# Optimization experiments

Hardware: AMD Instinct MI355X
Metric: run time of the kernel (lower is better)

The kernel has to match this reference:

```python
import jax, jax.numpy as jnp
import numpy as np

# --- module hyperparameters (init_kwargs) ---
IN_CH = 512
OUT_CH = 512
NUM_HEADS = 8
MODES = 64
LQ = 4096
LKV = 4096
E = IN_CH // NUM_HEADS      # per-head input dim = 64
EO = OUT_CH // NUM_HEADS    # per-head output dim = 64
B = 16

# mode_select_method='lowest' -> lowest-frequency modes, sorted (deterministic)
INDEX_Q = np.arange(min(MODES, LQ // 2))    # [Mq]
INDEX_KV = np.arange(min(MODES, LKV // 2))  # [Mkv]
SCALE = 1.0 / (IN_CH * OUT_CH)


def setup_inputs() -> dict:
    key = jax.random.key(0)
    kq, kk, kv, kw1, kw2 = jax.random.split(key, 5)
    return {
        "q": jax.random.normal(kq, (B, LQ, NUM_HEADS, E), jnp.float32),
        "k": jax.random.normal(kk, (B, LKV, NUM_HEADS, E), jnp.float32),
        "v": jax.random.normal(kv, (B, LKV, NUM_HEADS, E), jnp.float32),
        "weights1": SCALE * jax.random.normal(kw1, (NUM_HEADS, E, EO, len(INDEX_Q)), jnp.float32),
        "weights2": SCALE * jax.random.normal(kw2, (NUM_HEADS, E, EO, len(INDEX_Q)), jnp.float32),
    }


def reference(q, k, v, weights1, weights2):
    # q: [B, Lq, H, E]; k, v: [B, Lkv, H, E] (v is computed-but-unused in the
    # original forward; kept for signature fidelity).
    Bq, Lq, H, _ = q.shape
    xq = jnp.transpose(q, (0, 2, 3, 1))  # [B, H, E, Lq]
    xk = jnp.transpose(k, (0, 2, 3, 1))  # [B, H, E, Lkv]

    # rFFT along time, then gather the selected frequency modes
    xq_ft = jnp.fft.rfft(xq, axis=-1)[..., INDEX_Q]    # [B, H, E, Mq] complex
    xk_ft = jnp.fft.rfft(xk, axis=-1)[..., INDEX_KV]   # [B, H, E, Mkv] complex

    # complex cross-attention over modes (contract head-dim E)
    xqk = jnp.einsum('bhex,bhey->bhxy', xq_ft, xk_ft)  # [B, H, Mq, Mkv]
    # tanh applied independently to real/imag parts (as in compl activation)
    xqk = jax.lax.complex(jnp.tanh(xqk.real), jnp.tanh(xqk.imag))

    xqkv = jnp.einsum('bhxy,bhey->bhex', xqk, xk_ft)   # [B, H, E, Mq]

    w = jax.lax.complex(weights1, weights2)            # [H, E, EO, Mq]
    xqkvw = jnp.einsum('bhex,heox->bhox', xqkv, w)     # [B, H, EO, Mq]

    # scatter selected modes back into full half-spectrum, inverse FFT
    out_ft = jnp.zeros((Bq, H, EO, Lq // 2 + 1), jnp.complex64)
    out_ft = out_ft.at[..., INDEX_Q].set(xqkvw)
    out = jnp.fft.irfft(out_ft, n=Lq, axis=-1)         # [B, H, EO, Lq]

    out = jnp.transpose(out, (0, 3, 1, 2)) / (IN_CH * OUT_CH)  # [B, Lq, H, EO]
    return out
```

## Files before the change

kernel.cpp:

```cpp
#include <hip/hip_runtime.h>
#include <math.h>


constexpr float TWOPI_L = 1.5339807878856412e-3f;

typedef __attribute__((ext_vector_type(8))) short short8;
typedef __attribute__((ext_vector_type(4))) float f32x4;

__device__ __forceinline__ unsigned short f2bf(float f) {
    unsigned int u = __builtin_bit_cast(unsigned int, f);
    unsigned int r = (u + 0x7fffu + ((u >> 16) & 1u)) >> 16;
    return (unsigned short)r;
}
__device__ __forceinline__ float bf2f(unsigned short h) {
    unsigned int u = ((unsigned int)h) << 16;
    return __builtin_bit_cast(float, u);
}
__device__ __forceinline__ unsigned int cvtpk(float a, float b) {
    unsigned int r;
    asm("v_cvt_pk_bf16_f32 %0, %1, %2" : "=v"(r) : "v"(a), "v"(b));
    return r;
}
__device__ __forceinline__ void gld16(const float* g, void* l) {
    __builtin_amdgcn_global_load_lds(
        (const __attribute__((address_space(1))) void*)(g),
        (__attribute__((address_space(3))) void*)(l),
        16, 0, 0);
}
#define MSKR(r) (((((r) & 7)) << 1) | ((((r) >> 3)) & 1))

__global__ __launch_bounds__(256) void k0_twiddle(unsigned short* __restrict__ Whi,
                                                  unsigned short* __restrict__ Wlo) {
    const int idx = blockIdx.x * 256 + threadIdx.x;
    const int kt = idx >> 9;
    const int rb = (idx >> 6) & 7;
    const int l15 = (idx >> 2) & 15;
    const int lg = idx & 3;
    const int r_tab = rb * 16 + l15;
    int m, c;
    if (r_tab < 64) { m = (r_tab >> 1) * 2;              c = r_tab & 1; }
    else            { m = (((r_tab - 64) >> 1) * 2) + 1; c = r_tab & 1; }
    const int addr = (kt * 8 + rb) * 512 + l15 * 32 + lg * 8;
    unsigned short hbuf[8], lbuf[8];
#pragma unroll
    for (int j = 0; j < 8; ++j) {
        const int t = kt * 32 + lg * 8 + j;
        float sv, cv;
        sincosf((float)((m * t) & 4095) * TWOPI_L, &sv, &cv);
        const float v = c ? -sv : cv;
        const unsigned short hi = f2bf(v);
        hbuf[j] = hi;
        lbuf[j] = f2bf(v - bf2f(hi));
    }
    *(uint4*)(Whi + addr) = *(uint4*)hbuf;
    *(uint4*)(Wlo + addr) = *(uint4*)lbuf;
}

__global__ __launch_bounds__(256) void k0_basis(unsigned short* __restrict__ basis) {
    const int idx = blockIdx.x * 256 + threadIdx.x;
    const int p0 = idx << 2;
    const int t = p0 >> 6;
    unsigned int pk[4];
#pragma unroll
    for (int j = 0; j < 4; ++j) {
        const int m = (p0 & 63) + j;
        float sv, cv;
        sincosf((float)((m * t) & 4095) * TWOPI_L, &sv, &cv);
        const float c = (m == 0) ? 1.0f : 2.0f * cv;
        const float s = (m == 0) ? 0.0f : -2.0f * sv;
        pk[j] = (unsigned int)f2bf(c) | ((unsigned int)f2bf(s) << 16);
    }
    *(uint4*)(basis + (size_t)t * 128u + ((p0 & 63) << 1)) =
        make_uint4(pk[0], pk[1], pk[2], pk[3]);
}

__global__ __launch_bounds__(256, 2) void k1_mfma(const float* __restrict__ q,
                                                  const float* __restrict__ kin,
                                                  const unsigned short* __restrict__ Whi,
                                                  const unsigned short* __restrict__ Wlo,
                                                  float* __restrict__ Xq, float* __restrict__ Xk,
                                                  float* __restrict__ Pq, float* __restrict__ Pk)
{
    __shared__ float raw[3][64][64];
    __shared__ unsigned short xT[4][64][40];

    const int tid = threadIdx.x;
    const int bid = blockIdx.x;
    const int bh = bid >> 3, src = (bid >> 2) & 1, seg = bid & 3;
    const int b = bh >> 3, h = bh & 7;
    const float* __restrict__ x = src ? kin : q;
    const float* xb = x + (size_t)b * 2097152u + (size_t)h * 64u;

    const int wid = tid >> 6, lane = tid & 63;
    const int l15 = lane & 15, lg = lane >> 4;
    const int fp = (tid & 15) * 2;
    const int eqs = tid >> 4;
    const int sel = (wid >> 1) * 2;

    f32x4 acc[2][4];
#pragma unroll
    for (int mt = 0; mt < 2; ++mt)
#pragma unroll
        for (int nt = 0; nt < 4; ++nt)
            acc[mt][nt] = (f32x4){0.f, 0.f, 0.f, 0.f};

#define K1_STAGE(IT, BUF) do {                                                  \
    const int t0_ = (seg * 16 + ((IT) & 15)) * 32;                              \
    float* rbase_ = &raw[BUF][0][0];                                            \
    _Pragma("unroll")                                                           \
    for (int j = 0; j < 4; ++j) {                                               \
        const int c_ = wid * 4 + j;                                             \
        const int rl_ = 4 * c_ + (lane >> 4);                                   \
        const int t_ = t0_ + (rl_ & 31) + ((rl_ >> 5) << 11);                   \
        const int sq_ = (lane & 15) ^ MSKR(rl_);                                \
        gld16(xb + (size_t)t_ * 512u + (size_t)(sq_ * 4), rbase_ + c_ * 256);   \
    }                                                                           \
} while (0)

#define K1_ALOAD(IT, AH, AL) do {                                               \
    const int ksg_ = seg * 16 + ((IT) & 15);                                    \
    _Pragma("unroll")                                                           \
    for (int mt = 0; mt < 2; ++mt) {                                            \
        const size_t o_ = (size_t)((ksg_ * 8 + (wid * 2 + mt)) * 512 + l15 * 32 + lg * 8); \
        AH[mt] = *(const short8*)(Whi + o_);                                    \
        AL[mt] = *(const short8*)(Wlo + o_);                                    \
    }                                                                           \
} while (0)

#define K1_CONVERT(BUF) do {                                                    \
    const float* rb_ = &raw[BUF][0][0];                                         \
    float rs[16];                                                               \
    *(f32x4*)&rs[0]  = *(const f32x4*)(rb_ + (fp     ) * 64 + ((eqs ^ MSKR(fp))      * 4)); \
    *(f32x4*)&rs[4]  = *(const f32x4*)(rb_ + (fp + 1 ) * 64 + ((eqs ^ MSKR(fp + 1))  * 4)); \
    *(f32x4*)&rs[8]  = *(const f32x4*)(rb_ + (fp + 32) * 64 + ((eqs ^ MSKR(fp + 32)) * 4)); \
    *(f32x4*)&rs[12] = *(const f32x4*)(rb_ + (fp + 33) * 64 + ((eqs ^ MSKR(fp + 33)) * 4)); \
    _Pragma("unroll")                                                           \
    for (int ee = 0; ee < 4; ++ee) {                                            \
        const float a0 = rs[ee], a1 = rs[4 + ee];                               \
        const float c0 = rs[8 + ee], c1 = rs[12 + ee];                          \
        const float xp0 = a0 + c0, xp1 = a1 + c1;                               \
        const float xm0 = a0 - c0, xm1 = a1 - c1;                               \
        const int e_ = eqs * 4 + ee;                                            \
        const unsigned int php = cvtpk(xp0, xp1);                               \
        const float ph0 = __builtin_bit_cast(float, php << 16);                 \
        const float ph1 = __builtin_bit_cast(float, php & 0xffff0000u);         \
        const unsigned int plp = cvtpk(xp0 - ph0, xp1 - ph1);                   \
        const unsigned int mhp = cvtpk(xm0, xm1);                               \
        const float mh0 = __builtin_bit_cast(float, mhp << 16);                 \
        const float mh1 = __builtin_bit_cast(float, mhp & 0xffff0000u);         \
        const unsigned int mlp = cvtpk(xm0 - mh0, xm1 - mh1);                   \
        *(unsigned int*)&xT[0][e_][fp] = php;                                   \
        *(unsigned int*)&xT[1][e_][fp] = plp;                                   \
        *(unsigned int*)&xT[2][e_][fp] = mhp;                                   \
        *(unsigned int*)&xT[3][e_][fp] = mlp;                                   \
    }                                                                           \
} while (0)

#define K1_MFMA(AH, AL) do {                                                    \
    const unsigned short* sh = &xT[sel][0][0];                                  \
    const unsigned short* sl = &xT[sel + 1][0][0];                              \
    _Pragma("unroll")                                                           \
    for (int nt = 0; nt < 4; ++nt) {                                            \
        const int ri = (nt * 16 + l15) * 40 + 8 * lg;                           \
        const short8 Bh = *(const short8*)(sh + ri);                            \
        const short8 Bl = *(const short8*)(sl + ri);                            \
        _Pragma("unroll")                                                       \
        for (int mt = 0; mt < 2; ++mt)                                          \
            acc[mt][nt] = __builtin_amdgcn_mfma_f32_16x16x32_bf16(AH[mt], Bh, acc[mt][nt], 0, 0, 0); \
        _Pragma("unroll")                                                       \
        for (int mt = 0; mt < 2; ++mt)                                          \
            acc[mt][nt] = __builtin_amdgcn_mfma_f32_16x16x32_bf16(AH[mt], Bl, acc[mt][nt], 0, 0, 0); \
        _Pragma("unroll")                                                       \
        for (int mt = 0; mt < 2; ++mt)                                          \
            acc[mt][nt] = __builtin_amdgcn_mfma_f32_16x16x32_bf16(AL[mt], Bh, acc[mt][nt], 0, 0, 0); \
    }                                                                           \
} while (0)

    short8 AhA[2], AlA[2], AhB[2], AlB[2];
    K1_STAGE(0, 0);
    K1_ALOAD(0, AhA, AlA);
    K1_STAGE(1, 1);

    for (int itp = 0; itp < 8; ++itp) {
        const int it0 = 2 * itp;
        const int be = it0 % 3, bo = (it0 + 1) % 3;
        const int bs1 = (it0 + 2) % 3, bs2 = (it0 + 3) % 3;
        K1_ALOAD(it0 + 1, AhB, AlB);
        K1_STAGE(it0 + 2, bs1);
        __builtin_amdgcn_sched_barrier(0);
        asm volatile("s_waitcnt vmcnt(12)\n\ts_barrier" ::: "memory");
        K1_CONVERT(be);
        asm volatile("s_waitcnt lgkmcnt(0)\n\ts_barrier" ::: "memory");
        K1_MFMA(AhA, AlA);
        K1_ALOAD(it0 + 2, AhA, AlA);
        K1_STAGE(it0 + 3, bs2);
        __builtin_amdgcn_sched_barrier(0);
        asm volatile("s_waitcnt vmcnt(12)\n\ts_barrier" ::: "memory");
        K1_CONVERT(bo);
        asm volatile("s_waitcnt lgkmcnt(0)\n\ts_barrier" ::: "memory");
        K1_MFMA(AhB, AlB);
    }
    asm volatile("s_waitcnt vmcnt(0)" ::: "memory");

#undef K1_MFMA
#undef K1_CONVERT
#undef K1_ALOAD
#undef K1_STAGE

    float* Xd;
    if (seg == 0) Xd = src ? Xk : Xq;
    else          Xd = (src ? Pk : Pq) + (size_t)(seg - 1) * 1048576u;
    Xd += (size_t)bh * 8192u;
    const int oddw = wid >> 1;
    const int wb = wid & 1;
#pragma unroll
    for (int mt = 0; mt < 2; ++mt) {
        const int r0 = (wb * 2 + mt) * 32 + 8 * lg + 2 * oddw;
#pragma unroll
        for (int nt = 0; nt < 4; ++nt) {
            const int e = nt * 16 + l15;
            *(float2*)(Xd + (size_t)e * 128u + r0) =
                make_float2(acc[mt][nt][0], acc[mt][nt][1]);
            *(float2*)(Xd + (size_t)e * 128u + r0 + 4) =
                make_float2(acc[mt][nt][2], acc[mt][nt][3]);
        }
    }
}

__global__ __launch_bounds__(256) void k1_reduce(float* __restrict__ Xq, const float* __restrict__ Pq,
                                                 float* __restrict__ Xk, const float* __restrict__ Pk) {
    const int i = blockIdx.x * 256 + threadIdx.x;
    float4* a = (float4*)Xq;
    float4* c = (float4*)Xk;
    float4 v = a[i], w = c[i];
#pragma unroll
    for (int s = 0; s < 3; ++s) {
        const float4 p = ((const float4*)(Pq + (size_t)s * 1048576u))[i];
        const float4 r = ((const float4*)(Pk + (size_t)s * 1048576u))[i];
        v.x += p.x; v.y += p.y; v.z += p.z; v.w += p.w;
        w.x += r.x; w.y += r.y; w.z += r.z; w.w += r.w;
    }
    a[i] = v;
    c[i] = w;
}

__global__ __launch_bounds__(256) void k2a_p1(const float* __restrict__ Xq,
                                              const float* __restrict__ Xk,
                                              float* __restrict__ P)
{
    const int blk = blockIdx.x;
    const int bh = blk >> 2, xt = blk & 3;
    __shared__ float sQ[64 * 32];
    __shared__ float sK[64 * 128];
    const int tid = threadIdx.x;
    const float* Xqb = Xq + (size_t)bh * 8192u;
    const float* Xkb = Xk + (size_t)bh * 8192u;

#pragma unroll
    for (int p = 0; p < 2; ++p) {
        const int f4 = tid + p * 256;
        const int row = f4 >> 3, c4 = f4 & 7;
        *(float4*)&sQ[row * 32 + c4 * 4] = *(const float4*)(Xqb + row * 128 + xt * 32 + c4 * 4);
    }
#pragma unroll
    for (int p = 0; p < 8; ++p) {
        const int f4 = tid + p * 256;
        *(float4*)&sK[f4 * 4] = *(const float4*)(Xkb + f4 * 4);
    }
    __syncthreads();

    const int xg = tid & 15, yg = tid >> 4;
    float aR[4] = {0.f, 0.f, 0.f, 0.f}, aI[4] = {0.f, 0.f, 0.f, 0.f};
#pragma unroll 8
    for (int e = 0; e < 64; ++e) {
        const float2 qv = *(const float2*)&sQ[e * 32 + 2 * xg];
        const float4 k0 = *(const float4*)&sK[e * 128 + 8 * yg];
        const float4 k1v = *(const float4*)&sK[e * 128 + 8 * yg + 4];
        aR[0] += qv.x * k0.x - qv.y * k0.y;   aI[0] += qv.x * k0.y + qv.y * k0.x;
        aR[1] += qv.x * k0.z - qv.y * k0.w;   aI[1] += qv.x * k0.w + qv.y * k0.z;
        aR[2] += qv.x * k1v.x - qv.y * k1v.y; aI[2] += qv.x * k1v.y + qv.y * k1v.x;
        aR[3] += qv.x * k1v.z - qv.y * k1v.w; aI[3] += qv.x * k1v.w + qv.y * k1v.z;
    }
    float* Pb = P + (size_t)bh * 8192u;
    const int x_abs = xt * 16 + xg;
#pragma unroll
    for (int j = 0; j < 4; ++j) {
        const int y = 4 * yg + j;
        *(float2*)(Pb + (size_t)y * 128u + 2 * x_abs) =
            make_float2(tanhf(aR[j]), tanhf(aI[j]));
    }
}

__global__ __launch_bounds__(256) void k2b_p3(const float* __restrict__ P,
                                              const float* __restrict__ Xk,
                                              float* __restrict__ PVG)
{
    const int blk = blockIdx.x;
    const int bh = blk >> 2, et = blk & 3;
    const int b = bh >> 3, h = bh & 7;
    __shared__ float sP[64 * 128];
    __shared__ float sKe[16 * 132];
    const int tid = threadIdx.x;
    const float* Pb = P + (size_t)bh * 8192u;
    const float* Xkb = Xk + (size_t)bh * 8192u + (size_t)(et * 16) * 128u;

#pragma unroll
    for (int p = 0; p < 8; ++p) {
        const int f4 = tid + p * 256;
        *(float4*)&sP[f4 * 4] = *(const float4*)(Pb + f4 * 4);
    }
#pragma unroll
    for (int p = 0; p < 2; ++p) {
        const int f4 = tid + p * 256;
        const int row = f4 >> 5, c4 = f4 & 31;
        *(float4*)&sKe[row * 132 + c4 * 4] = *(const float4*)(Xkb + row * 128 + c4 * 4);
    }
    __syncthreads();

    const int xg = tid & 15, el = tid >> 4;
    float aR[4] = {0.f, 0.f, 0.f, 0.f}, aI[4] = {0.f, 0.f, 0.f, 0.f};
#pragma unroll 8
    for (int y = 0; y < 64; ++y) {
        const float2 kv = *(const float2*)&sKe[el * 132 + 2 * y];
        const float4 p0 = *(const float4*)&sP[y * 128 + 8 * xg];
        const float4 p1 = *(const float4*)&sP[y * 128 + 8 * xg + 4];
        aR[0] += p0.x * kv.x - p0.y * kv.y;   aI[0] += p0.x * kv.y + p0.y * kv.x;
        aR[1] += p0.z * kv.x - p0.w * kv.y;   aI[1] += p0.z * kv.y + p0.w * kv.x;
        aR[2] += p1.x * kv.x - p1.y * kv.y;   aI[2] += p1.x * kv.y + p1.y * kv.x;
        aR[3] += p1.z * kv.x - p1.w * kv.y;   aI[3] += p1.z * kv.y + p1.w * kv.x;
    }
    const int e_abs = et * 16 + el;
    float* base = PVG + (size_t)h * 131072u;
#pragma unroll
    for (int j = 0; j < 4; ++j) {
        const int m = 4 * xg + j;
        base[(size_t)m * 2048u + 0u    + (size_t)b * 64u + e_abs] = aR[j];
        base[(size_t)m * 2048u + 1024u + (size_t)b * 64u + e_abs] = aI[j];
    }
}

__global__ __launch_bounds__(256) void kwt(const float* __restrict__ w1,
                                           const float* __restrict__ w2,
                                           float* __restrict__ wT)
{
    const int blk = blockIdx.x;
    const int h = blk >> 6, e = blk & 63;
    __shared__ float s1[64][65];
    __shared__ float s2[64][65];
    const int tid = threadIdx.x;
    const float* w1b = w1 + (size_t)(h * 64 + e) * 4096u;
    const float* w2b = w2 + (size_t)(h * 64 + e) * 4096u;
#pragma unroll
    for (int p = 0; p < 4; ++p) {
        const int f4 = tid + p * 256;
        const int o = f4 >> 4, m4 = (f4 & 15) * 4;
        *(float4*)&s1[o][m4] = *(const float4*)(w1b + f4 * 4);
        *(float4*)&s2[o][m4] = *(const float4*)(w2b + f4 * 4);
    }
    __syncthreads();
    float* dstb = wT + ((size_t)(h * 64) * 64u + (size_t)e) * 128u;
#pragma unroll
    for (int p = 0; p < 8; ++p) {
        const int f4 = tid + p * 256;
        const int m = f4 >> 5, c4 = f4 & 31;
        const int o = c4 * 2;
        const float4 v = make_float4(s1[o][m], s2[o][m], s1[o + 1][m], s2[o + 1][m]);
        *(float4*)(dstb + (size_t)m * 8192u + c4 * 4) = v;
    }
}

__global__ __launch_bounds__(256) void k2c_p4(const float* __restrict__ PVG,
                                              const float* __restrict__ wT,
                                              unsigned short* __restrict__ XWThi,
                                              unsigned short* __restrict__ XWTlo)
{
    const int blk = blockIdx.x;
    const int h = blk >> 6, m = blk & 63;
    __shared__ float sA[32 * 68];
    __shared__ float sW[64 * 128];
    const int tid = threadIdx.x;
    const float* Ab = PVG + (size_t)h * 131072u + (size_t)m * 2048u;
    const float* Wb = wT + ((size_t)h * 64u + m) * 8192u;

#pragma unroll
    for (int p = 0; p < 2; ++p) {
        const int f4 = tid + p * 256;
        const int row = f4 >> 4, e0 = (f4 & 15) * 4;
        *(float4*)&sA[row * 68 + e0] = *(const float4*)(Ab + row * 64 + e0);
    }
#pragma unroll
    for (int p = 0; p < 8; ++p) {
        const int f4 = tid + p * 256;
        *(float4*)&sW[f4 * 4] = *(const float4*)(Wb + f4 * 4);
    }
    __syncthreads();

    const int og = tid & 15, b = tid >> 4;
    float aR[4] = {0.f, 0.f, 0.f, 0.f}, aI[4] = {0.f, 0.f, 0.f, 0.f};
#pragma unroll 8
    for (int e = 0; e < 64; ++e) {
        const float pR = sA[b * 68 + e];
        const float pI = sA[(16 + b) * 68 + e];
        const float4 w0 = *(const float4*)&sW[e * 128 + 8 * og];
        const float4 w1v = *(const float4*)&sW[e * 128 + 8 * og + 4];
        aR[0] += pR * w0.x - pI * w0.y;   aI[0] += pR * w0.y + pI * w0.x;
        aR[1] += pR * w0.z - pI * w0.w;   aI[1] += pR * w0.w + pI * w0.z;
        aR[2] += pR * w1v.x - pI * w1v.y; aI[2] += pR * w1v.y + pI * w1v.x;
        aR[3] += pR * w1v.z - pI * w1v.w; aI[3] += pR * w1v.w + pI * w1v.z;
    }
    const int bh = b * 8 + h;
    unsigned short* Th = XWThi + (size_t)bh * 8192u;
    unsigned short* Tl = XWTlo + (size_t)bh * 8192u;
#pragma unroll
    for (int j = 0; j < 4; ++j) {
        const int o = 4 * og + j;
        const unsigned int hp = cvtpk(aR[j], aI[j]);
        const float hR = __builtin_bit_cast(float, hp << 16);
        const float hI = __builtin_bit_cast(float, hp & 0xffff0000u);
        const unsigned int lp = cvtpk(aR[j] - hR, aI[j] - hI);
        *(unsigned int*)(Th + (size_t)o * 128u + 2 * m) = hp;
        *(unsigned int*)(Tl + (size_t)o * 128u + 2 * m) = lp;
    }
}

__global__ __launch_bounds__(256, 3) void k3_mfma(const unsigned short* __restrict__ basis,
                                                  const unsigned short* __restrict__ XWThi,
                                                  const unsigned short* __restrict__ XWTlo,
                                                  float* __restrict__ out)
{
    const int bid = blockIdx.x;
    const int bh = bid >> 4, tc = bid & 15;
    const int b = bh >> 3, h = bh & 7;
    const int tid = threadIdx.x;
    const int wid = tid >> 6, lane = tid & 63;
    const int l15 = lane & 15, lg = lane >> 4;

    const int t0 = tc * 256 + wid * 64;
    const unsigned short* Th = XWThi + (size_t)bh * 8192u;
    const unsigned short* Tl = XWTlo + (size_t)bh * 8192u;

    f32x4 acc[4][4];
#pragma unroll
    for (int mt = 0; mt < 4; ++mt)
#pragma unroll
        for (int nt = 0; nt < 4; ++nt)
            acc[mt][nt] = (f32x4){0.f, 0.f, 0.f, 0.f};

#pragma unroll
    for (int ks = 0; ks < 4; ++ks) {
        const int ko = ks * 32 + 8 * lg;
        short8 A[4], Bh[4], Bl[4];
#pragma unroll
        for (int mt = 0; mt < 4; ++mt)
            A[mt] = *(const short8*)(basis + (size_t)(t0 + mt * 16 + l15) * 128u + ko);
#pragma unroll
        for (int nt = 0; nt < 4; ++nt) {
            Bh[nt] = *(const short8*)(Th + (size_t)(nt * 16 + l15) * 128u + ko);
            Bl[nt] = *(const short8*)(Tl + (size_t)(nt * 16 + l15) * 128u + ko);
        }
#pragma unroll
        for (int mt = 0; mt < 4; ++mt)
#pragma unroll
            for (int nt = 0; nt < 4; ++nt)
                acc[mt][nt] = __builtin_amdgcn_mfma_f32_16x16x32_bf16(A[mt], Bh[nt], acc[mt][nt], 0, 0, 0);
#pragma unroll
        for (int mt = 0; mt < 4; ++mt)
#pragma unroll
            for (int nt = 0; nt < 4; ++nt)
                acc[mt][nt] = __builtin_amdgcn_mfma_f32_16x16x32_bf16(A[mt], Bl[nt], acc[mt][nt], 0, 0, 0);
    }

    const float scale = 9.313225746154785e-10f;
#pragma unroll
    for (int mt = 0; mt < 4; ++mt)
#pragma unroll
        for (int nt = 0; nt < 4; ++nt) {
            const int o = nt * 16 + l15;
#pragma unroll
            for (int j = 0; j < 4; ++j) {
                const int t = t0 + mt * 16 + 4 * lg + j;
                out[((size_t)(b * 4096 + t) * 8u + (size_t)h) * 64u + o] = acc[mt][nt][j] * scale;
            }
        }
}

extern "C" void kernel_launch(void* const* d_in, const int* in_sizes, int n_in,
                              void* d_out, int out_size, void* d_ws, size_t ws_size,
                              hipStream_t stream) {
    (void)in_sizes; (void)n_in; (void)out_size; (void)ws_size;
    const float* q  = (const float*)d_in[0];
    const float* k  = (const float*)d_in[1];
    const float* w1 = (const float*)d_in[3];
    const float* w2 = (const float*)d_in[4];
    float* out = (float*)d_out;

    float* ws = (float*)d_ws;
    float* Xq = ws;
    float* Xk = ws + 1048576;
    unsigned short* XWThi = (unsigned short*)(ws + 2097152);
    unsigned short* XWTlo = XWThi + 1048576;
    unsigned short* basis = (unsigned short*)ws;

    unsigned short* Whi = (unsigned short*)out;
    unsigned short* Wlo = Whi + 262144;
    float* Pq  = out + 524288;
    float* Pk  = out + 3670016;
    float* P   = out + 16777216;
    float* wT  = out + 17825792;
    float* PVG = out + 22020096;

    hipLaunchKernelGGL(k0_twiddle, dim3(128),  dim3(256), 0, stream, Whi, Wlo);
    hipLaunchKernelGGL(k1_mfma,    dim3(1024), dim3(256), 0, stream, q, k, Whi, Wlo, Xq, Xk, Pq, Pk);
    hipLaunchKernelGGL(k1_reduce,  dim3(1024), dim3(256), 0, stream, Xq, Pq, Xk, Pk);
    hipLaunchKernelGGL(k2a_p1,     dim3(512),  dim3(256), 0, stream, Xq, Xk, P);
    hipLaunchKernelGGL(k0_basis,   dim3(256),  dim3(256), 0, stream, basis);
    hipLaunchKernelGGL(k2b_p3,     dim3(512),  dim3(256), 0, stream, P, Xk, PVG);
    hipLaunchKernelGGL(kwt,        dim3(512),  dim3(256), 0, stream, w1, w2, wT);
    hipLaunchKernelGGL(k2c_p4,     dim3(512),  dim3(256), 0, stream, PVG, wT, XWThi, XWTlo);
    hipLaunchKernelGGL(k3_mfma,    dim3(2048), dim3(256), 0, stream, basis, XWThi, XWTlo, out);
}
```

Measured before the change: 206.4 us.

## Merge setup kernels and halve k1 time-split to cut launches and partial sums

Merges the twiddle-table and weight-transpose kernels into one launch, and folds the basis generation into the k2b kernel as extra blocks. This drops the launch count from nine to seven. It also changes the forward-DFT kernel to split time into 2 segments instead of 4, so each block loops twice as long and there is one partial buffer instead of three. That means less reduction traffic, but only half as many blocks (512) to fill the GPU.

```diff
diff --git a/kernel.cpp b/kernel.cpp
--- a/kernel.cpp
+++ b/kernel.cpp
@@ -29,49 +29,63 @@
 }
 #define MSKR(r) (((((r) & 7)) << 1) | ((((r) >> 3)) & 1))
 
-__global__ __launch_bounds__(256) void k0_twiddle(unsigned short* __restrict__ Whi,
-                                                  unsigned short* __restrict__ Wlo) {
-    const int idx = blockIdx.x * 256 + threadIdx.x;
-    const int kt = idx >> 9;
-    const int rb = (idx >> 6) & 7;
-    const int l15 = (idx >> 2) & 15;
-    const int lg = idx & 3;
-    const int r_tab = rb * 16 + l15;
-    int m, c;
-    if (r_tab < 64) { m = (r_tab >> 1) * 2;              c = r_tab & 1; }
-    else            { m = (((r_tab - 64) >> 1) * 2) + 1; c = r_tab & 1; }
-    const int addr = (kt * 8 + rb) * 512 + l15 * 32 + lg * 8;
-    unsigned short hbuf[8], lbuf[8];
-#pragma unroll
-    for (int j = 0; j < 8; ++j) {
-        const int t = kt * 32 + lg * 8 + j;
-        float sv, cv;
-        sincosf((float)((m * t) & 4095) * TWOPI_L, &sv, &cv);
-        const float v = c ? -sv : cv;
-        const unsigned short hi = f2bf(v);
-        hbuf[j] = hi;
-        lbuf[j] = f2bf(v - bf2f(hi));
-    }
-    *(uint4*)(Whi + addr) = *(uint4*)hbuf;
-    *(uint4*)(Wlo + addr) = *(uint4*)lbuf;
-}
-
-__global__ __launch_bounds__(256) void k0_basis(unsigned short* __restrict__ basis) {
-    const int idx = blockIdx.x * 256 + threadIdx.x;
-    const int p0 = idx << 2;
-    const int t = p0 >> 6;
-    unsigned int pk[4];
-#pragma unroll
-    for (int j = 0; j < 4; ++j) {
-        const int m = (p0 & 63) + j;
-        float sv, cv;
-        sincosf((float)((m * t) & 4095) * TWOPI_L, &sv, &cv);
-        const float c = (m == 0) ? 1.0f : 2.0f * cv;
-        const float s = (m == 0) ? 0.0f : -2.0f * sv;
-        pk[j] = (unsigned int)f2bf(c) | ((unsigned int)f2bf(s) << 16);
-    }
-    *(uint4*)(basis + (size_t)t * 128u + ((p0 & 63) << 1)) =
-        make_uint4(pk[0], pk[1], pk[2], pk[3]);
+__global__ __launch_bounds__(256) void kprep(unsigned short* __restrict__ Whi,
+                                             unsigned short* __restrict__ Wlo,
+                                             const float* __restrict__ w1,
+                                             const float* __restrict__ w2,
+                                             float* __restrict__ wT)
+{
+    __shared__ float s1[64][65];
+    __shared__ float s2[64][65];
+    const int blk = blockIdx.x;
+    const int tid = threadIdx.x;
+    if (blk < 128) {
+        const int idx = blk * 256 + tid;
+        const int kt = idx >> 9;
+        const int rb = (idx >> 6) & 7;
+        const int l15 = (idx >> 2) & 15;
+        const int lg = idx & 3;
+        const int r_tab = rb * 16 + l15;
+        int m, c;
+        if (r_tab < 64) { m = (r_tab >> 1) * 2;              c = r_tab & 1; }
+        else            { m = (((r_tab - 64) >> 1) * 2) + 1; c = r_tab & 1; }
+        const int addr = (kt * 8 + rb) * 512 + l15 * 32 + lg * 8;
+        unsigned short hbuf[8], lbuf[8];
+#pragma unroll
+        for (int j = 0; j < 8; ++j) {
+            const int t = kt * 32 + lg * 8 + j;
+            float sv, cv;
+            sincosf((float)((m * t) & 4095) * TWOPI_L, &sv, &cv);
+            const float v = c ? -sv : cv;
+            const unsigned short hi = f2bf(v);
+            hbuf[j] = hi;
+            lbuf[j] = f2bf(v - bf2f(hi));
+        }
+        *(uint4*)(Whi + addr) = *(uint4*)hbuf;
+        *(uint4*)(Wlo + addr) = *(uint4*)lbuf;
+    } else {
+        const int wblk = blk - 128;
+        const int h = wblk >> 6, e = wblk & 63;
+        const float* w1b = w1 + (size_t)(h * 64 + e) * 4096u;
+        const float* w2b = w2 + (size_t)(h * 64 + e) * 4096u;
+#pragma unroll
+        for (int p = 0; p < 4; ++p) {
+            const int f4 = tid + p * 256;
+            const int o = f4 >> 4, m4 = (f4 & 15) * 4;
+            *(float4*)&s1[o][m4] = *(const float4*)(w1b + f4 * 4);
+            *(float4*)&s2[o][m4] = *(const float4*)(w2b + f4 * 4);
+        }
+        __syncthreads();
+        float* dstb = wT + ((size_t)(h * 64) * 64u + (size_t)e) * 128u;
+#pragma unroll
+        for (int p = 0; p < 8; ++p) {
+            const int f4 = tid + p * 256;
+            const int m = f4 >> 5, c4 = f4 & 31;
+            const int o = c4 * 2;
+            const float4 v = make_float4(s1[o][m], s2[o][m], s1[o + 1][m], s2[o + 1][m]);
+            *(float4*)(dstb + (size_t)m * 8192u + c4 * 4) = v;
+        }
+    }
 }
 
 __global__ __launch_bounds__(256, 2) void k1_mfma(const float* __restrict__ q,
@@ -86,7 +100,7 @@
 
     const int tid = threadIdx.x;
     const int bid = blockIdx.x;
-    const int bh = bid >> 3, src = (bid >> 2) & 1, seg = bid & 3;
+    const int bh = bid >> 2, src = (bid >> 1) & 1, seg = bid & 1;
     const int b = bh >> 3, h = bh & 7;
     const float* __restrict__ x = src ? kin : q;
     const float* xb = x + (size_t)b * 2097152u + (size_t)h * 64u;
@@ -105,7 +119,7 @@
             acc[mt][nt] = (f32x4){0.f, 0.f, 0.f, 0.f};
 
 #define K1_STAGE(IT, BUF) do {                                                  \
-    const int t0_ = (seg * 16 + ((IT) & 15)) * 32;                              \
+    const int t0_ = (seg * 32 + ((IT) & 31)) * 32;                              \
     float* rbase_ = &raw[BUF][0][0];                                            \
     _Pragma("unroll")                                                           \
     for (int j = 0; j < 4; ++j) {                                               \
@@ -118,7 +132,7 @@
 } while (0)
 
 #define K1_ALOAD(IT, AH, AL) do {                                               \
-    const int ksg_ = seg * 16 + ((IT) & 15);                                    \
+    const int ksg_ = seg * 32 + ((IT) & 31);                                    \
     _Pragma("unroll")                                                           \
     for (int mt = 0; mt < 2; ++mt) {                                            \
         const size_t o_ = (size_t)((ksg_ * 8 + (wid * 2 + mt)) * 512 + l15 * 32 + lg * 8); \
@@ -181,7 +195,7 @@
     K1_ALOAD(0, AhA, AlA);
     K1_STAGE(1, 1);
 
-    for (int itp = 0; itp < 8; ++itp) {
+    for (int itp = 0; itp < 16; ++itp) {
         const int it0 = 2 * itp;
         const int be = it0 % 3, bo = (it0 + 1) % 3;
         const int bs1 = (it0 + 2) % 3, bs2 = (it0 + 3) % 3;
@@ -209,7 +223,7 @@
 
     float* Xd;
     if (seg == 0) Xd = src ? Xk : Xq;
-    else          Xd = (src ? Pk : Pq) + (size_t)(seg - 1) * 1048576u;
+    else          Xd = src ? Pk : Pq;
     Xd += (size_t)bh * 8192u;
     const int oddw = wid >> 1;
     const int wb = wid & 1;
@@ -233,13 +247,10 @@
     float4* a = (float4*)Xq;
     float4* c = (float4*)Xk;
     float4 v = a[i], w = c[i];
-#pragma unroll
-    for (int s = 0; s < 3; ++s) {
-        const float4 p = ((const float4*)(Pq + (size_t)s * 1048576u))[i];
-        const float4 r = ((const float4*)(Pk + (size_t)s * 1048576u))[i];
-        v.x += p.x; v.y += p.y; v.z += p.z; v.w += p.w;
-        w.x += r.x; w.y += r.y; w.z += r.z; w.w += r.w;
-    }
+    const float4 p = ((const float4*)Pq)[i];
+    const float4 r = ((const float4*)Pk)[i];
+    v.x += p.x; v.y += p.y; v.z += p.z; v.w += p.w;
+    w.x += r.x; w.y += r.y; w.z += r.z; w.w += r.w;
     a[i] = v;
     c[i] = w;
 }
@@ -291,16 +302,35 @@
     }
 }
 
-__global__ __launch_bounds__(256) void k2b_p3(const float* __restrict__ P,
-                                              const float* __restrict__ Xk,
-                                              float* __restrict__ PVG)
+__global__ __launch_bounds__(256) void k2b_basis(const float* __restrict__ P,
+                                                 const float* __restrict__ Xk,
+                                                 float* __restrict__ PVG,
+                                                 unsigned short* __restrict__ basis)
 {
+    __shared__ float sP[64 * 128];
+    __shared__ float sKe[16 * 132];
     const int blk = blockIdx.x;
+    const int tid = threadIdx.x;
+    if (blk >= 512) {
+        const int idx = (blk - 512) * 256 + tid;
+        const int p0 = idx << 2;
+        const int t = p0 >> 6;
+        unsigned int pk[4];
+#pragma unroll
+        for (int j = 0; j < 4; ++j) {
+            const int m = (p0 & 63) + j;
+            float sv, cv;
+            sincosf((float)((m * t) & 4095) * TWOPI_L, &sv, &cv);
+            const float c = (m == 0) ? 1.0f : 2.0f * cv;
+            const float s = (m == 0) ? 0.0f : -2.0f * sv;
+            pk[j] = (unsigned int)f2bf(c) | ((unsigned int)f2bf(s) << 16);
+        }
+        *(uint4*)(basis + (size_t)t * 128u + ((p0 & 63) << 1)) =
+            make_uint4(pk[0], pk[1], pk[2], pk[3]);
+        return;
+    }
     const int bh = blk >> 2, et = blk & 3;
     const int b = bh >> 3, h = bh & 7;
-    __shared__ float sP[64 * 128];
-    __shared__ float sKe[16 * 132];
-    const int tid = threadIdx.x;
     const float* Pb = P + (size_t)bh * 8192u;
     const float* Xkb = Xk + (size_t)bh * 8192u + (size_t)(et * 16) * 128u;
 
@@ -336,36 +366,6 @@
         const int m = 4 * xg + j;
         base[(size_t)m * 2048u + 0u    + (size_t)b * 64u + e_abs] = aR[j];
         base[(size_t)m * 2048u + 1024u + (size_t)b * 64u + e_abs] = aI[j];
-    }
-}
-
-__global__ __launch_bounds__(256) void kwt(const float* __restrict__ w1,
-                                           const float* __restrict__ w2,
-                                           float* __restrict__ wT)
-{
-    const int blk = blockIdx.x;
-    const int h = blk >> 6, e = blk & 63;
-    __shared__ float s1[64][65];
-    __shared__ float s2[64][65];
-    const int tid = threadIdx.x;
-    const float* w1b = w1 + (size_t)(h * 64 + e) * 4096u;
-    const float* w2b = w2 + (size_t)(h * 64 + e) * 4096u;
-#pragma unroll
-    for (int p = 0; p < 4; ++p) {
-        const int f4 = tid + p * 256;
-        const int o = f4 >> 4, m4 = (f4 & 15) * 4;
-        *(float4*)&s1[o][m4] = *(const float4*)(w1b + f4 * 4);
-        *(float4*)&s2[o][m4] = *(const float4*)(w2b + f4 * 4);
-    }
-    __syncthreads();
-    float* dstb = wT + ((size_t)(h * 64) * 64u + (size_t)e) * 128u;
-#pragma unroll
-    for (int p = 0; p < 8; ++p) {
-        const int f4 = tid + p * 256;
-        const int m = f4 >> 5, c4 = f4 & 31;
-        const int o = c4 * 2;
-        const float4 v = make_float4(s1[o][m], s2[o][m], s1[o + 1][m], s2[o + 1][m]);
-        *(float4*)(dstb + (size_t)m * 8192u + c4 * 4) = v;
     }
 }
 
@@ -504,18 +504,16 @@
     unsigned short* Whi = (unsigned short*)out;
     unsigned short* Wlo = Whi + 262144;
     float* Pq  = out + 524288;
-    float* Pk  = out + 3670016;
+    float* Pk  = out + 1572864;
     float* P   = out + 16777216;
     float* wT  = out + 17825792;
     float* PVG = out + 22020096;
 
-    hipLaunchKernelGGL(k0_twiddle, dim3(128),  dim3(256), 0, stream, Whi, Wlo);
-    hipLaunchKernelGGL(k1_mfma,    dim3(1024), dim3(256), 0, stream, q, k, Whi, Wlo, Xq, Xk, Pq, Pk);
-    hipLaunchKernelGGL(k1_reduce,  dim3(1024), dim3(256), 0, stream, Xq, Pq, Xk, Pk);
-    hipLaunchKernelGGL(k2a_p1,     dim3(512),  dim3(256), 0, stream, Xq, Xk, P);
-    hipLaunchKernelGGL(k0_basis,   dim3(256),  dim3(256), 0, stream, basis);
-    hipLaunchKernelGGL(k2b_p3,     dim3(512),  dim3(256), 0, stream, P, Xk, PVG);
-    hipLaunchKernelGGL(kwt,        dim3(512),  dim3(256), 0, stream, w1, w2, wT);
-    hipLaunchKernelGGL(k2c_p4,     dim3(512),  dim3(256), 0, stream, PVG, wT, XWThi, XWTlo);
-    hipLaunchKernelGGL(k3_mfma,    dim3(2048), dim3(256), 0, stream, basis, XWThi, XWTlo, out);
-}
+    hipLaunchKernelGGL(kprep,     dim3(640),  dim3(256), 0, stream, Whi, Wlo, w1, w2, wT);
+    hipLaunchKernelGGL(k1_mfma,   dim3(512),  dim3(256), 0, stream, q, k, Whi, Wlo, Xq, Xk, Pq, Pk);
+    hipLaunchKernelGGL(k1_reduce, dim3(1024), dim3(256), 0, stream, Xq, Pq, Xk, Pk);
+    hipLaunchKernelGGL(k2a_p1,    dim3(512),  dim3(256), 0, stream, Xq, Xk, P);
+    hipLaunchKernelGGL(k2b_basis, dim3(768),  dim3(256), 0, stream, P, Xk, PVG, basis);
+    hipLaunchKernelGGL(k2c_p4,    dim3(512),  dim3(256), 0, stream, PVG, wT, XWThi, XWTlo);
+    hipLaunchKernelGGL(k3_mfma,   dim3(2048), dim3(256), 0, stream, basis, XWThi, XWTlo, out);
+}
```

Result: faster. 190.4 us (-7.7%).
